# Kernel optimization log

Measured on AMD Instinct MI355X. Metric: run time of the kernel, lower is better.

Reference implementation:

```python
import jax, jax.numpy as jnp
import numpy as np


def setup_inputs() -> dict:
    key = jax.random.key(0)
    k1, k2, k3 = jax.random.split(key, 3)
    B, S, D = 4, 2048, 4096
    C, E = 8, 8  # num_clusters, experts per cluster
    hidden_states = jax.random.normal(k1, (B, S, D), dtype=jnp.float32)
    W_cluster = jax.random.normal(k2, (C, D), dtype=jnp.float32) * 0.02
    W_experts = jax.random.normal(k3, (C, E, D), dtype=jnp.float32) * 0.02
    expert_ids = jnp.arange(C * E, dtype=jnp.int64).reshape(C, E)
    return {"hidden_states": hidden_states, "W_cluster": W_cluster,
            "W_experts": W_experts, "expert_ids": expert_ids}


def reference(hidden_states, W_cluster, W_experts, expert_ids):
    # hidden_states: [B, S, D]; W_cluster: [C, D]; W_experts: [C, E, D]; expert_ids: [C, E]
    B, S, D = hidden_states.shape
    C, E, _ = W_experts.shape
    num_total = C * E
    x = hidden_states.reshape(-1, D)                      # [T, D]
    T = x.shape[0]
    # First-level: token-level top-1 cluster routing (cluster_token_routing=True).
    # softmax is monotone, so argmax over logits == argmax over softmax weights.
    cluster_logits = x @ W_cluster.T                      # [T, C]
    cluster_idx = jnp.argmax(cluster_logits, axis=-1)     # [T]
    # Second-level: expert logits for every cluster, then gather the chosen cluster's.
    all_logits = jnp.einsum('td,ced->tce', x, W_experts)  # [T, C, E]
    rows = jnp.arange(T)
    sel_logits = all_logits[rows, cluster_idx]            # [T, E]
    cols = expert_ids[cluster_idx]                        # [T, E] global expert slots
    neg_min = jnp.finfo(hidden_states.dtype).min
    routing = jnp.full((T, num_total), neg_min, dtype=hidden_states.dtype)
    routing = routing.at[rows[:, None], cols].set(sel_logits)
    return routing.reshape(B, S, num_total)
```

## Files before the change

kernel.cpp:

```cpp
#include <hip/hip_runtime.h>
#include <cfloat>

#define DDIM 4096
#define NCLUS 8
#define NEXP 8
#define NOUT 64
#define NW 72
#define NCOL 80
#define FILL_BITS 0xFF7F0000u
#define WS_BYTES (8 * 16 * 5 * 64 * 16)

typedef float floatx4 __attribute__((ext_vector_type(4)));
typedef short bf16x8 __attribute__((ext_vector_type(8)));

__device__ __forceinline__ short bfh(float f) {
  return (short)(__float_as_uint(f) >> 16);
}
__device__ __forceinline__ bf16x8 pack8(const float4& a, const float4& b) {
  bf16x8 r;
  r[0] = bfh(a.x); r[1] = bfh(a.y); r[2] = bfh(a.z); r[3] = bfh(a.w);
  r[4] = bfh(b.x); r[5] = bfh(b.y); r[6] = bfh(b.z); r[7] = bfh(b.w);
  return r;
}

__global__ __launch_bounds__(256) void k_pack(const float* __restrict__ Wc,
                                              const float* __restrict__ We,
                                              bf16x8* __restrict__ ws) {
  const int gtid = blockIdx.x * 256 + threadIdx.x;
  const int frag = gtid >> 6;
  const int lane = gtid & 63;
  const int w = frag / 80;
  const int rem = frag % 80;
  const int s = rem / 5;
  const int ct = rem % 5;
  const int row = ct * 16 + (lane & 15);
  const int k = w * 512 + s * 32 + (lane >> 4) * 8;

  float4 b0 = {0.f, 0.f, 0.f, 0.f}, b1 = {0.f, 0.f, 0.f, 0.f};
  if (row < NW) {
    const float* rp = (row < NCLUS) ? (Wc + (size_t)row * DDIM)
                                    : (We + (size_t)(row - NCLUS) * DDIM);
    b0 = *(const float4*)(rp + k);
    b1 = *(const float4*)(rp + k + 4);
  }
  ws[gtid] = pack8(b0, b1);
}

template <bool USE_WS>
__global__ __launch_bounds__(512, 4) void k_mfma(const float* __restrict__ x,
                                                 const float* __restrict__ Wc,
                                                 const float* __restrict__ We,
                                                 const int* __restrict__ eids32,
                                                 const bf16x8* __restrict__ bws,
                                                 float* __restrict__ out) {
  __shared__ float s_acc[8][16 * NCOL];

  const int tid = threadIdx.x;
  const int lane = tid & 63;
  const int wave = tid >> 6;
  const int tile0 = blockIdx.x * 16;

  const int m = lane & 15;
  const int q = lane >> 4;
  const int kw = wave * 512 + q * 8;

  const float* xrow = x + (size_t)(tile0 + m) * DDIM + kw;
  const bf16x8* bbase = USE_WS ? (bws + (size_t)wave * 16 * 5 * 64 + lane) : nullptr;

  floatx4 acc[5];
#pragma unroll
  for (int ct = 0; ct < 5; ++ct) acc[ct] = (floatx4){0.f, 0.f, 0.f, 0.f};

  float4 pa0 = *(const float4*)(xrow);
  float4 pa1 = *(const float4*)(xrow + 4);
  bf16x8 pb[5];
  float4 pb0[5], pb1[5];
#pragma unroll
  for (int ct = 0; ct < 5; ++ct) {
    if (USE_WS) {
      pb[ct] = bbase[ct * 64];
    } else {
      const int wrow = ct * 16 + m;
      pb0[ct] = (float4){0.f, 0.f, 0.f, 0.f};
      pb1[ct] = (float4){0.f, 0.f, 0.f, 0.f};
      if (wrow < NW) {
        const float* bp = (wrow < NCLUS) ? (Wc + (size_t)wrow * DDIM)
                                         : (We + (size_t)(wrow - NCLUS) * DDIM);
        pb0[ct] = *(const float4*)(bp + kw);
        pb1[ct] = *(const float4*)(bp + kw + 4);
      }
    }
  }

#pragma unroll
  for (int step = 0; step < 16; ++step) {
    const float4 ca0 = pa0, ca1 = pa1;
    bf16x8 cb[5];
#pragma unroll
    for (int ct = 0; ct < 5; ++ct)
      cb[ct] = USE_WS ? pb[ct] : pack8(pb0[ct], pb1[ct]);

    if (step < 15) {
      const int kb = (step + 1) * 32;
      pa0 = *(const float4*)(xrow + kb);
      pa1 = *(const float4*)(xrow + kb + 4);
#pragma unroll
      for (int ct = 0; ct < 5; ++ct) {
        if (USE_WS) {
          pb[ct] = bbase[((step + 1) * 5 + ct) * 64];
        } else {
          const int wrow = ct * 16 + m;
          if (wrow < NW) {
            const float* bp = (wrow < NCLUS) ? (Wc + (size_t)wrow * DDIM)
                                             : (We + (size_t)(wrow - NCLUS) * DDIM);
            pb0[ct] = *(const float4*)(bp + kw + kb);
            pb1[ct] = *(const float4*)(bp + kw + kb + 4);
          }
        }
      }
    }

    const bf16x8 af = pack8(ca0, ca1);
#pragma unroll
    for (int ct = 0; ct < 5; ++ct)
      acc[ct] = __builtin_amdgcn_mfma_f32_16x16x32_bf16(af, cb[ct], acc[ct], 0, 0, 0);
  }

#pragma unroll
  for (int ct = 0; ct < 5; ++ct)
#pragma unroll
    for (int r = 0; r < 4; ++r)
      s_acc[wave][(q * 4 + r) * NCOL + ct * 16 + m] = acc[ct][r];
  __syncthreads();

  for (int i = tid; i < 16 * NCOL; i += 512) {
    float s = s_acc[0][i];
#pragma unroll
    for (int w = 1; w < 8; ++w) s += s_acc[w][i];
    s_acc[0][i] = s;
  }
  __syncthreads();

  const int is64 = (eids32[1] == 0) ? 1 : 0;
  const float fillv = __uint_as_float(FILL_BITS);
  for (int idx = tid; idx < 16 * NOUT; idx += 512) {
    const int tok = idx >> 6;
    const int col = idx & 63;
    const float* P = &s_acc[0][tok * NCOL];
    float best = P[0];
    int c = 0;
#pragma unroll
    for (int cc = 1; cc < NCLUS; ++cc)
      if (P[cc] > best) { best = P[cc]; c = cc; }
    float val = fillv;
#pragma unroll
    for (int e = 0; e < NEXP; ++e) {
      const int slot = c * NEXP + e;
      const int ce = is64 ? eids32[slot << 1] : eids32[slot];
      if (ce == col) val = P[NCLUS + slot];
    }
    out[(size_t)(tile0 + tok) * NOUT + col] = val;
  }
}

extern "C" void kernel_launch(void* const* d_in, const int* in_sizes, int n_in,
                              void* d_out, int out_size, void* d_ws, size_t ws_size,
                              hipStream_t stream) {
  const float* x = (const float*)d_in[0];
  const float* Wc = (const float*)d_in[1];
  const float* We = (const float*)d_in[2];
  const int* eids = (const int*)d_in[3];
  float* out = (float*)d_out;

  const int T = in_sizes[0] / DDIM;

  if (ws_size >= (size_t)WS_BYTES) {
    bf16x8* bws = (bf16x8*)d_ws;
    k_pack<<<160, 256, 0, stream>>>(Wc, We, bws);
    k_mfma<true><<<T / 16, 512, 0, stream>>>(x, Wc, We, eids, bws, out);
  } else {
    k_mfma<false><<<T / 16, 512, 0, stream>>>(x, Wc, We, eids, nullptr, out);
  }
}
```

Before: 208.0 us.

## Process 32 tokens per block to reuse weight fragments across two row tiles

Each block now computes two 16-token tiles, sharing every loaded weight fragment between two MFMA accumulator sets. This halves weight fragment loads per token and doubles the x loads in flight per thread. In exchange the launch bound drops to 2 blocks per CU, register use grows, and the grid is halved. The epilogue reduction runs twice through shared memory with an extra barrier.

```diff
diff --git a/kernel.cpp b/kernel.cpp
--- a/kernel.cpp
+++ b/kernel.cpp
@@ -47,7 +47,7 @@
 }
 
 template <bool USE_WS>
-__global__ __launch_bounds__(512, 4) void k_mfma(const float* __restrict__ x,
+__global__ __launch_bounds__(512, 2) void k_mfma(const float* __restrict__ x,
                                                  const float* __restrict__ Wc,
                                                  const float* __restrict__ We,
                                                  const int* __restrict__ eids32,
@@ -58,21 +58,27 @@
   const int tid = threadIdx.x;
   const int lane = tid & 63;
   const int wave = tid >> 6;
-  const int tile0 = blockIdx.x * 16;
+  const int tile0 = blockIdx.x * 32;
 
   const int m = lane & 15;
   const int q = lane >> 4;
   const int kw = wave * 512 + q * 8;
 
-  const float* xrow = x + (size_t)(tile0 + m) * DDIM + kw;
+  const float* xrow0 = x + (size_t)(tile0 + m) * DDIM + kw;
+  const float* xrow1 = xrow0 + (size_t)16 * DDIM;
   const bf16x8* bbase = USE_WS ? (bws + (size_t)wave * 16 * 5 * 64 + lane) : nullptr;
 
-  floatx4 acc[5];
-#pragma unroll
-  for (int ct = 0; ct < 5; ++ct) acc[ct] = (floatx4){0.f, 0.f, 0.f, 0.f};
-
-  float4 pa0 = *(const float4*)(xrow);
-  float4 pa1 = *(const float4*)(xrow + 4);
+  floatx4 acc0[5], acc1[5];
+#pragma unroll
+  for (int ct = 0; ct < 5; ++ct) {
+    acc0[ct] = (floatx4){0.f, 0.f, 0.f, 0.f};
+    acc1[ct] = (floatx4){0.f, 0.f, 0.f, 0.f};
+  }
+
+  float4 pa0 = *(const float4*)(xrow0);
+  float4 pa1 = *(const float4*)(xrow0 + 4);
+  float4 pc0 = *(const float4*)(xrow1);
+  float4 pc1 = *(const float4*)(xrow1 + 4);
   bf16x8 pb[5];
   float4 pb0[5], pb1[5];
 #pragma unroll
@@ -94,7 +100,7 @@
 
 #pragma unroll
   for (int step = 0; step < 16; ++step) {
-    const float4 ca0 = pa0, ca1 = pa1;
+    const float4 ca0 = pa0, ca1 = pa1, cc0 = pc0, cc1 = pc1;
     bf16x8 cb[5];
 #pragma unroll
     for (int ct = 0; ct < 5; ++ct)
@@ -102,8 +108,10 @@
 
     if (step < 15) {
       const int kb = (step + 1) * 32;
-      pa0 = *(const float4*)(xrow + kb);
-      pa1 = *(const float4*)(xrow + kb + 4);
+      pa0 = *(const float4*)(xrow0 + kb);
+      pa1 = *(const float4*)(xrow0 + kb + 4);
+      pc0 = *(const float4*)(xrow1 + kb);
+      pc1 = *(const float4*)(xrow1 + kb + 4);
 #pragma unroll
       for (int ct = 0; ct < 5; ++ct) {
         if (USE_WS) {
@@ -120,46 +128,57 @@
       }
     }
 
-    const bf16x8 af = pack8(ca0, ca1);
-#pragma unroll
-    for (int ct = 0; ct < 5; ++ct)
-      acc[ct] = __builtin_amdgcn_mfma_f32_16x16x32_bf16(af, cb[ct], acc[ct], 0, 0, 0);
-  }
-
-#pragma unroll
-  for (int ct = 0; ct < 5; ++ct)
-#pragma unroll
-    for (int r = 0; r < 4; ++r)
-      s_acc[wave][(q * 4 + r) * NCOL + ct * 16 + m] = acc[ct][r];
-  __syncthreads();
-
-  for (int i = tid; i < 16 * NCOL; i += 512) {
-    float s = s_acc[0][i];
-#pragma unroll
-    for (int w = 1; w < 8; ++w) s += s_acc[w][i];
-    s_acc[0][i] = s;
-  }
-  __syncthreads();
+    const bf16x8 af0 = pack8(ca0, ca1);
+    const bf16x8 af1 = pack8(cc0, cc1);
+#pragma unroll
+    for (int ct = 0; ct < 5; ++ct) {
+      acc0[ct] = __builtin_amdgcn_mfma_f32_16x16x32_bf16(af0, cb[ct], acc0[ct], 0, 0, 0);
+      acc1[ct] = __builtin_amdgcn_mfma_f32_16x16x32_bf16(af1, cb[ct], acc1[ct], 0, 0, 0);
+    }
+  }
 
   const int is64 = (eids32[1] == 0) ? 1 : 0;
   const float fillv = __uint_as_float(FILL_BITS);
-  for (int idx = tid; idx < 16 * NOUT; idx += 512) {
-    const int tok = idx >> 6;
-    const int col = idx & 63;
-    const float* P = &s_acc[0][tok * NCOL];
-    float best = P[0];
-    int c = 0;
-#pragma unroll
-    for (int cc = 1; cc < NCLUS; ++cc)
-      if (P[cc] > best) { best = P[cc]; c = cc; }
-    float val = fillv;
-#pragma unroll
-    for (int e = 0; e < NEXP; ++e) {
-      const int slot = c * NEXP + e;
-      const int ce = is64 ? eids32[slot << 1] : eids32[slot];
-      if (ce == col) val = P[NCLUS + slot];
-    }
-    out[(size_t)(tile0 + tok) * NOUT + col] = val;
+
+#pragma unroll
+  for (int half = 0; half < 2; ++half) {
+    if (half) __syncthreads();
+
+#pragma unroll
+    for (int ct = 0; ct < 5; ++ct)
+#pragma unroll
+      for (int r = 0; r < 4; ++r) {
+        const floatx4& a = half ? acc1[ct] : acc0[ct];
+        s_acc[wave][(q * 4 + r) * NCOL + ct * 16 + m] = a[r];
+      }
+    __syncthreads();
+
+    for (int i = tid; i < 16 * NCOL; i += 512) {
+      float s = s_acc[0][i];
+#pragma unroll
+      for (int w = 1; w < 8; ++w) s += s_acc[w][i];
+      s_acc[0][i] = s;
+    }
+    __syncthreads();
+
+    for (int idx = tid; idx < 16 * NOUT; idx += 512) {
+      const int tok = idx >> 6;
+      const int col = idx & 63;
+      const float* P = &s_acc[0][tok * NCOL];
+      float best = P[0];
+      int c = 0;
+#pragma unroll
+      for (int cc = 1; cc < NCLUS; ++cc)
+        if (P[cc] > best) { best = P[cc]; c = cc; }
+      float val = fillv;
+#pragma unroll
+      for (int e = 0; e < NEXP; ++e) {
+        const int slot = c * NEXP + e;
+        const int ce = is64 ? eids32[slot << 1] : eids32[slot];
+        if (ce == col) val = P[NCLUS + slot];
+      }
+      out[(size_t)(tile0 + half * 16 + tok) * NOUT + col] = val;
+    }
   }
 }
 
@@ -177,8 +196,8 @@
   if (ws_size >= (size_t)WS_BYTES) {
     bf16x8* bws = (bf16x8*)d_ws;
     k_pack<<<160, 256, 0, stream>>>(Wc, We, bws);
-    k_mfma<true><<<T / 16, 512, 0, stream>>>(x, Wc, We, eids, bws, out);
+    k_mfma<true><<<T / 32, 512, 0, stream>>>(x, Wc, We, eids, bws, out);
   } else {
-    k_mfma<false><<<T / 16, 512, 0, stream>>>(x, Wc, We, eids, nullptr, out);
-  }
-}
+    k_mfma<false><<<T / 32, 512, 0, stream>>>(x, Wc, We, eids, nullptr, out);
+  }
+}
```

After: 205.5 us. About the same (-1.2%).
